# Kernel optimization log

Measured on AMD Instinct MI355X. Metric: run time of the kernel, lower is better.

Reference implementation:

```python
import jax, jax.numpy as jnp
import numpy as np

D_EMB = 512
TIME_HORIZON = 1024.0
SEP_FOR_GRIDS = 1.0


def _sinusoid(x, D):
    # x: [..., D], already divided by the 10000^(2*(i//2)/D) position vector.
    # even dims -> sin, odd dims -> cos (matches the torch in-place slicing)
    idx = jnp.arange(D)
    return jnp.where(idx % 2 == 0, jnp.sin(x), jnp.cos(x))


def setup_inputs() -> dict:
    key = jax.random.key(0)
    k1, k2, k3 = jax.random.split(key, 3)
    T, B, L, D = 2, 16, 2048, D_EMB
    # positive event timestamps in (0, time_horizon); strictly nonzero so pad mask == valid-by-length mask logic stays simple
    times = jax.random.uniform(k1, (T, B, L), dtype=jnp.float32) * TIME_HORIZON
    type_emb = jax.random.normal(k2, (T, D), dtype=jnp.float32)  # nn.Embedding weight
    real_len = jax.random.randint(k3, (T, B), 1, L)              # ragged valid lengths per type per sample
    return {"times": times, "type_emb": type_emb, "real_len": real_len}


def reference(times, type_emb, real_len):
    T, B, L = times.shape
    D = type_emb.shape[1]
    pos = jnp.power(jnp.float32(10000.0), 2.0 * (jnp.arange(D) // 2) / D)  # [D]

    # per-event embedding = (time sinusoid + type embedding) masked by nonzero-pad
    pad = (times != 0)[..., None]                                         # [T,B,L,1]
    emb = (_sinusoid(times[..., None] / pos, D) + type_emb[:, None, None, :]) * pad  # [T,B,L,D]
    emb = emb.transpose(1, 0, 2, 3).reshape(B, T * L, D)                  # [B, T*L, D]

    # grid queries: sinusoidal encoding of grid mid-times
    G = int(TIME_HORIZON / SEP_FOR_GRIDS)
    mid = (jnp.arange(G, dtype=jnp.float32) + 0.5) * SEP_FOR_GRIDS        # [G]
    q = _sinusoid(mid[:, None] / pos, D)                                  # [G,D]

    # dot-product scores vs grid queries, scaled
    scores = jnp.einsum('bnd,gd->bng', emb, q) / jnp.sqrt(jnp.float32(D)) # [B,T*L,G]

    # ragged validity: only first real_len events of each type block take part in softmax
    valid = jnp.arange(L)[None, None, :] < real_len[:, :, None]           # [T,B,L]
    valid = valid.transpose(1, 0, 2).reshape(B, T * L)                    # [B,T*L]

    # masked softmax over events (dim of concatenated valid events), weighted sum of embeddings
    w = jax.nn.softmax(jnp.where(valid[:, :, None], scores, -jnp.inf), axis=1)  # [B,T*L,G]
    return jnp.einsum('bng,bnd->bgd', w, emb)                             # [B,G,D]
```

## Files before the change

### kernel.cpp

```cpp
#include <hip/hip_runtime.h>
#include <hip/hip_bf16.h>
#include <math.h>

#define TT 2
#define BB 16
#define LL 2048
#define NN 4096
#define DD 512
#define GG 1024
#define SCALE 0.044194173824159216f
#define LOG2E 1.4426950408889634f
#define QSCL (SCALE * LOG2E)
#define C_IP 0.051905126482615036f

typedef unsigned short ushort_t;
typedef short short8 __attribute__((ext_vector_type(8)));
typedef float f32x4 __attribute__((ext_vector_type(4)));

__device__ __forceinline__ float inv_pos_f(int dhalf) {
    return exp2f(-C_IP * (float)dhalf);
}
__device__ __forceinline__ unsigned short f2b(float f) {
    union { float f; unsigned u; } x; x.f = f;
    unsigned r = x.u + 0x7fffu + ((x.u >> 16) & 1u);
    return (unsigned short)(r >> 16);
}
__device__ __forceinline__ float b2f(unsigned short u) {
    union { unsigned u; float f; } x; x.u = ((unsigned)u) << 16;
    return x.f;
}

__global__ void genT_kernel(const float* __restrict__ times,
                            const float* __restrict__ type_emb,
                            ushort_t* __restrict__ embT) {
    __shared__ float s_tm[64];
    __shared__ float s_te[DD];
    const int bid = blockIdx.x;
    const int b = bid >> 6;
    const int ntile = bid & 63;
    const int t = ntile >> 5;
    const int l0 = (ntile & 31) * 64;
    const int tid = threadIdx.x;

    if (tid < 64) s_tm[tid] = times[(size_t)(t * BB + b) * LL + l0 + tid];
    s_te[tid]       = type_emb[t * DD + tid];
    s_te[tid + 256] = type_emb[t * DD + tid + 256];
    __syncthreads();

    const int dsub = tid >> 3;
    const int nc = (tid & 7) * 8;
#pragma unroll 4
    for (int pass = 0; pass < 16; ++pass) {
        const int d = pass * 32 + dsub;
        const float ip = inv_pos_f(d >> 1);
        const float te = s_te[d];
        const bool use_cos = (d & 1);
        union { ushort_t us[8]; short8 v; } o;
#pragma unroll
        for (int j = 0; j < 8; ++j) {
            const float tm = s_tm[nc + j];
            const float th = tm * ip;
            const float v = use_cos ? __cosf(th) : __sinf(th);
            o.us[j] = f2b((v + te) * ((tm != 0.0f) ? 1.0f : 0.0f));
        }
        *reinterpret_cast<short8*>(
            embT + ((size_t)b * DD + d) * NN + (size_t)ntile * 64 + nc) = o.v;
    }
}

__global__ void ftab4_kernel(float* __restrict__ F4) {
    const int tid = threadIdx.x;
    const int e = blockIdx.x * 32 + (tid >> 3);
    const int jj = tid & 7;
    const float d0 = (float)e - 1024.0f;
    const float d1 = d0 + 1.0f;
    float F0 = 0.f, F1 = 0.f, D0 = 0.f, D1 = 0.f;
    for (int j = jj; j < 256; j += 8) {
        const float w = inv_pos_f(j);
        float s0, c0, s1, c1;
        __sincosf(d0 * w, &s0, &c0);
        __sincosf(d1 * w, &s1, &c1);
        F0 += c0; D0 -= w * s0;
        F1 += c1; D1 -= w * s1;
    }
#pragma unroll
    for (int off = 1; off < 8; off <<= 1) {
        F0 += __shfl_xor(F0, off, 64); F1 += __shfl_xor(F1, off, 64);
        D0 += __shfl_xor(D0, off, 64); D1 += __shfl_xor(D1, off, 64);
    }
    if (jj == 0) {
        const float cc = 3.f * (F1 - F0) - 2.f * D0 - D1;
        const float ee = 2.f * (F0 - F1) + D0 + D1;
        float4 v;
        v.x = F0 * QSCL; v.y = D0 * QSCL; v.z = cc * QSCL; v.w = ee * QSCL;
        reinterpret_cast<float4*>(F4)[e] = v;
    }
}

__global__ void gq_kernel(const float* __restrict__ type_emb, float* __restrict__ G) {
    const int g = blockIdx.x;
    const int tid = threadIdx.x;
    const float mid = (float)g + 0.5f;
    float a0 = 0.f, a1 = 0.f;
#pragma unroll
    for (int i = 0; i < 2; ++i) {
        const int d = i * 256 + tid;
        const float th = mid * inv_pos_f(d >> 1);
        const float v = (d & 1) ? cosf(th) : sinf(th);
        a0 += v * type_emb[d];
        a1 += v * type_emb[DD + d];
    }
#pragma unroll
    for (int off = 32; off; off >>= 1) {
        a0 += __shfl_xor(a0, off, 64);
        a1 += __shfl_xor(a1, off, 64);
    }
    __shared__ float r0[4], r1[4];
    const int wv = tid >> 6;
    if ((tid & 63) == 0) { r0[wv] = a0; r1[wv] = a1; }
    __syncthreads();
    if (tid == 0) {
        G[g]      = r0[0] + r0[1] + r0[2] + r0[3];
        G[GG + g] = r1[0] + r1[1] + r1[2] + r1[3];
    }
}

template <int NS>
__global__ __launch_bounds__(256, 2)
void attn5(const float* __restrict__ times,
           const ushort_t* __restrict__ embT,
           const float* __restrict__ Ft4,
           const float* __restrict__ Gt,
           const int* __restrict__ real_len,
           ushort_t* __restrict__ pO,
           float* __restrict__ pl) {
    __shared__ float4 sF[2048];
    __shared__ __align__(16) ushort_t sP[2][32 * 40];
    __shared__ float s_lred[2][32];

    constexpr int TPS = 128 / NS;
    const int idx = blockIdx.x;
    const int xcd = idx & 7;
    const int gt = (idx >> 3) & 31;
    const int hi = idx >> 8;
    const int b = xcd + ((hi & 1) << 3);
    const int s = hi >> 1;
    const int g0 = gt * 32;

    const int tid = threadIdx.x;
    const int lane = tid & 63;
    const int w = tid >> 6;
    const int l15 = lane & 15;
    const int quad = lane >> 4;
    const int mt1 = w >> 1;
    const int gt1 = w & 1;

    const int gme = g0 + gt1 * 16 + l15;
    const float gmid = (float)gme + 0.5f;
    const float c0 = Gt[gme] * QSCL - 4.0f;
    const float c1 = Gt[GG + gme] * QSCL - 4.0f;

    const ushort_t* embTB = embT + (size_t)b * DD * NN;

    const int rl0 = real_len[b];
    const int rl1 = real_len[BB + b];
    const int e0 = (rl0 + 31) >> 5;
    const int e1 = (rl1 + 31) >> 5;
    const int first = s * TPS;
    int count;
    if (first < 64) count = min(max(e0 - first, 0), TPS);
    else            count = min(max(64 + e1 - first, 0), TPS);

    f32x4 accO[8][2];
#pragma unroll
    for (int i = 0; i < 8; ++i) { accO[i][0] = (f32x4)0.f; accO[i][1] = (f32x4)0.f; }
    float ls = 0.f;

    short8 tf[8];
    auto prefetchT = [&](int nt) {
        const ushort_t* trow = embTB + (size_t)(w * 128 + l15) * NN + nt * 32 + quad * 8;
#pragma unroll
        for (int mt = 0; mt < 8; ++mt)
            tf[mt] = *reinterpret_cast<const short8*>(trow + (size_t)mt * 16 * NN);
    };
    auto times4 = [&](int nt) -> float4 {
        const int n = nt * 32 + mt1 * 16 + quad * 4;
        return *reinterpret_cast<const float4*>(
            times + (size_t)((n >> 11) * BB + b) * LL + (n & (LL - 1)));
    };

    float4 hv[4];
    float sr[4];
    auto gather = [&](float4 t4) {
        const float tt[4] = {t4.x, t4.y, t4.z, t4.w};
#pragma unroll
        for (int r = 0; r < 4; ++r) {
            const float u = (tt[r] - gmid) + 1024.0f;
            const int i = (int)u;
            sr[r] = u - (float)i;
            hv[r] = sF[i];
        }
    };

    if (count > 0) {
        const float4* Fg = reinterpret_cast<const float4*>(Ft4);
#pragma unroll
        for (int i = 0; i < 8; ++i) sF[tid + i * 256] = Fg[tid + i * 256];
        prefetchT(first);
        const float4 t40 = times4(first);
        __syncthreads();
        gather(t40);
    }
    float4 t4n;
    if (count > 1) t4n = times4(first + 1);

    for (int k = 0; k < count; ++k) {
        const int cur = first + k;
        const int buf = k & 1;

        const int nb = cur * 32 + mt1 * 16 + quad * 4;
        const int rl = (nb >= LL) ? rl1 : rl0;
        const float cc = (nb >= LL) ? c1 : c0;
        const int lb = nb & (LL - 1);
        float p[4];
#pragma unroll
        for (int r = 0; r < 4; ++r) {
            const float sv = sr[r];
            const float4 h = hv[r];
            const float Fv = h.x + sv * (h.y + sv * (h.z + sv * h.w));
            p[r] = (lb + r < rl) ? exp2f(Fv + cc) : 0.0f;
        }
        ls += (p[0] + p[1]) + (p[2] + p[3]);
        {
            union { unsigned short us[4]; unsigned long long u64; } pk;
            pk.us[0] = f2b(p[0]); pk.us[1] = f2b(p[1]); pk.us[2] = f2b(p[2]); pk.us[3] = f2b(p[3]);
            *reinterpret_cast<unsigned long long*>(
                sP[buf] + (gt1 * 16 + l15) * 40 + mt1 * 16 + quad * 4) = pk.u64;
        }

        asm volatile("s_waitcnt lgkmcnt(0)\n" ::: "memory");
        __builtin_amdgcn_s_barrier();

        if (k + 1 < count) {
            gather(t4n);
            if (k + 2 < count) t4n = times4(cur + 2);
        }

        {
            short8 bP0 = *reinterpret_cast<const short8*>(sP[buf] + l15 * 40 + quad * 8);
            short8 bP1 = *reinterpret_cast<const short8*>(sP[buf] + (16 + l15) * 40 + quad * 8);
            __builtin_amdgcn_s_setprio(1);
#pragma unroll
            for (int mt = 0; mt < 8; ++mt) {
                accO[mt][0] = __builtin_amdgcn_mfma_f32_16x16x32_bf16(tf[mt], bP0, accO[mt][0], 0, 0, 0);
                accO[mt][1] = __builtin_amdgcn_mfma_f32_16x16x32_bf16(tf[mt], bP1, accO[mt][1], 0, 0, 0);
            }
            __builtin_amdgcn_s_setprio(0);
        }
        if (k + 1 < count) prefetchT(cur + 1);
    }

    ls += __shfl_xor(ls, 16, 64);
    ls += __shfl_xor(ls, 32, 64);
    if (lane < 16) s_lred[mt1][gt1 * 16 + lane] = ls;
    __syncthreads();

    if (w == 0 && lane < 32)
        pl[((size_t)s * BB + b) * GG + g0 + lane] = s_lred[0][lane] + s_lred[1][lane];

    ushort_t* po = pO + (((size_t)s * BB + b) * GG) * DD;
#pragma unroll
    for (int mt = 0; mt < 8; ++mt) {
#pragma unroll
        for (int gtt = 0; gtt < 2; ++gtt) {
            union { unsigned short us[4]; unsigned long long u64; } pk;
            pk.us[0] = f2b(accO[mt][gtt][0]); pk.us[1] = f2b(accO[mt][gtt][1]);
            pk.us[2] = f2b(accO[mt][gtt][2]); pk.us[3] = f2b(accO[mt][gtt][3]);
            const int g = g0 + gtt * 16 + l15;
            const int d = w * 128 + mt * 16 + quad * 4;
            *reinterpret_cast<unsigned long long*>(po + (size_t)g * DD + d) = pk.u64;
        }
    }
}

template <int NS>
__global__ void combine3(const ushort_t* __restrict__ pO,
                         const float* __restrict__ pl,
                         float* __restrict__ out) {
    const size_t i4 = (size_t)blockIdx.x * 256 + threadIdx.x;
    const size_t base = i4 * 4;
    const size_t bg = base >> 9;
    float lsum = 0.f;
#pragma unroll
    for (int s = 0; s < NS; ++s) lsum += pl[(size_t)s * BB * GG + bg];
    const float inv = 1.0f / lsum;
    float o[4] = {0.f, 0.f, 0.f, 0.f};
#pragma unroll
    for (int s = 0; s < NS; ++s) {
        union { unsigned long long u64; unsigned short us[4]; } pk;
        pk.u64 = *reinterpret_cast<const unsigned long long*>(
            pO + (size_t)s * BB * GG * DD + base);
#pragma unroll
        for (int j = 0; j < 4; ++j) o[j] += b2f(pk.us[j]);
    }
    float4 v;
    v.x = o[0] * inv; v.y = o[1] * inv; v.z = o[2] * inv; v.w = o[3] * inv;
    *reinterpret_cast<float4*>(out + base) = v;
}

__global__ void emb_kernel(const float* __restrict__ times,
                           const float* __restrict__ type_emb,
                           ushort_t* __restrict__ emb) {
    const int row = blockIdx.x;
    const int b = row >> 12;
    const int n = row & (NN - 1);
    const int t = n >> 11;
    const int l = n & (LL - 1);
    const float tm = times[(size_t)(t * BB + b) * LL + l];
    const float pad = (tm != 0.0f) ? 1.0f : 0.0f;
    const int tid = threadIdx.x;
#pragma unroll
    for (int i = 0; i < 2; ++i) {
        int d = i * 256 + tid;
        float theta = tm * inv_pos_f(d >> 1);
        float v = (d & 1) ? cosf(theta) : sinf(theta);
        v = (v + type_emb[t * DD + d]) * pad;
        emb[(size_t)row * DD + d] = f2b(v);
    }
}
__global__ void qgrid_kernel(float* __restrict__ qbuf) {
    const int g = blockIdx.x;
    const int tid = threadIdx.x;
    const float mid = (float)g + 0.5f;
#pragma unroll
    for (int i = 0; i < 4; ++i) {
        int d = i * 128 + tid;
        float theta = mid * inv_pos_f(d >> 1);
        float v = (d & 1) ? cosf(theta) : sinf(theta);
        qbuf[(size_t)g * DD + d] = v;
    }
}
__global__ void attn_kernel(const ushort_t* __restrict__ emb,
                            const float* __restrict__ qbuf,
                            const int* __restrict__ real_len,
                            float* __restrict__ out) {
    __shared__ float s_lds[NN];
    __shared__ float q_s[DD];
    __shared__ float red[8];
    const int blk = blockIdx.x;
    const int b = blk >> 10;
    const int g = blk & (GG - 1);
    const int tid = threadIdx.x;
    const int lane = tid & 63;
    const int wave = tid >> 6;
    q_s[tid]       = qbuf[(size_t)g * DD + tid];
    q_s[tid + 256] = qbuf[(size_t)g * DD + tid + 256];
    __syncthreads();
    float qr[8];
#pragma unroll
    for (int j = 0; j < 8; ++j) qr[j] = q_s[lane * 8 + j];
    const unsigned int* embB =
        reinterpret_cast<const unsigned int*>(emb) + (size_t)b * NN * (DD / 2);
#pragma unroll 2
    for (int it = 0; it < NN / 4; ++it) {
        const int n = it * 4 + wave;
        const uint4 raw = *reinterpret_cast<const uint4*>(embB + (size_t)n * (DD / 2) + lane * 4);
        float sacc = 0.f;
        sacc = fmaf(__uint_as_float(raw.x << 16),         qr[0], sacc);
        sacc = fmaf(__uint_as_float(raw.x & 0xffff0000u), qr[1], sacc);
        sacc = fmaf(__uint_as_float(raw.y << 16),         qr[2], sacc);
        sacc = fmaf(__uint_as_float(raw.y & 0xffff0000u), qr[3], sacc);
        sacc = fmaf(__uint_as_float(raw.z << 16),         qr[4], sacc);
        sacc = fmaf(__uint_as_float(raw.z & 0xffff0000u), qr[5], sacc);
        sacc = fmaf(__uint_as_float(raw.w << 16),         qr[6], sacc);
        sacc = fmaf(__uint_as_float(raw.w & 0xffff0000u), qr[7], sacc);
#pragma unroll
        for (int off = 32; off; off >>= 1) sacc += __shfl_xor(sacc, off, 64);
        if (lane == 0) s_lds[n] = sacc * SCALE;
    }
    __syncthreads();
    const int rl0 = real_len[b];
    const int rl1 = real_len[BB + b];
    float m = -INFINITY;
    float sv[16];
#pragma unroll
    for (int i = 0; i < 16; ++i) {
        const int n = i * 256 + tid;
        float sc = s_lds[n];
        const int l = n & (LL - 1);
        const bool valid = l < ((n < LL) ? rl0 : rl1);
        sc = valid ? sc : -INFINITY;
        sv[i] = sc;
        m = fmaxf(m, sc);
    }
#pragma unroll
    for (int off = 32; off; off >>= 1) m = fmaxf(m, __shfl_xor(m, off, 64));
    if (lane == 0) red[wave] = m;
    __syncthreads();
    m = fmaxf(fmaxf(red[0], red[1]), fmaxf(red[2], red[3]));
    float lsum = 0.f;
#pragma unroll
    for (int i = 0; i < 16; ++i) {
        const int n = i * 256 + tid;
        const float e = expf(sv[i] - m);
        s_lds[n] = e;
        lsum += e;
    }
#pragma unroll
    for (int off = 32; off; off >>= 1) lsum += __shfl_xor(lsum, off, 64);
    if (lane == 0) red[4 + wave] = lsum;
    __syncthreads();
    const float inv_l = 1.0f / (red[4] + red[5] + red[6] + red[7]);
    float acc[8] = {0.f, 0.f, 0.f, 0.f, 0.f, 0.f, 0.f, 0.f};
#pragma unroll 2
    for (int kk = 0; kk < NN / 4; ++kk) {
        const int n = kk * 4 + wave;
        const float p = s_lds[n];
        const uint4 raw = *reinterpret_cast<const uint4*>(embB + (size_t)n * (DD / 2) + lane * 4);
        acc[0] = fmaf(p, __uint_as_float(raw.x << 16),         acc[0]);
        acc[1] = fmaf(p, __uint_as_float(raw.x & 0xffff0000u), acc[1]);
        acc[2] = fmaf(p, __uint_as_float(raw.y << 16),         acc[2]);
        acc[3] = fmaf(p, __uint_as_float(raw.y & 0xffff0000u), acc[3]);
        acc[4] = fmaf(p, __uint_as_float(raw.z << 16),         acc[4]);
        acc[5] = fmaf(p, __uint_as_float(raw.z & 0xffff0000u), acc[5]);
        acc[6] = fmaf(p, __uint_as_float(raw.w << 16),         acc[6]);
        acc[7] = fmaf(p, __uint_as_float(raw.w & 0xffff0000u), acc[7]);
    }
    __syncthreads();
    *reinterpret_cast<float4*>(&s_lds[wave * DD + lane * 8])     = make_float4(acc[0], acc[1], acc[2], acc[3]);
    *reinterpret_cast<float4*>(&s_lds[wave * DD + lane * 8 + 4]) = make_float4(acc[4], acc[5], acc[6], acc[7]);
    __syncthreads();
    {
        const int d0 = tid * 2;
        const float o0 = (s_lds[d0]     + s_lds[DD + d0]     + s_lds[2 * DD + d0]     + s_lds[3 * DD + d0])     * inv_l;
        const float o1 = (s_lds[d0 + 1] + s_lds[DD + d0 + 1] + s_lds[2 * DD + d0 + 1] + s_lds[3 * DD + d0 + 1]) * inv_l;
        *reinterpret_cast<float2*>(out + (size_t)blk * DD + d0) = make_float2(o0, o1);
    }
}

extern "C" void kernel_launch(void* const* d_in, const int* in_sizes, int n_in,
                              void* d_out, int out_size, void* d_ws, size_t ws_size,
                              hipStream_t stream) {
    const float* times    = (const float*)d_in[0];
    const float* type_emb = (const float*)d_in[1];
    const int*   real_len = (const int*)d_in[2];
    float* out = (float*)d_out;

    const size_t embTBytes = (size_t)BB * DD * NN * sizeof(ushort_t);
    const size_t tabBytes  = 64 * 1024;
    const size_t pOslice   = (size_t)BB * GG * DD * sizeof(ushort_t);
    const size_t plslice   = (size_t)BB * GG * sizeof(float);

    ushort_t* embT = (ushort_t*)d_ws;
    float* Ftab = (float*)((char*)d_ws + embTBytes);
    float* Gtab = (float*)((char*)d_ws + embTBytes + 32 * 1024);
    char* pbase = (char*)d_ws + embTBytes + tabBytes;

    auto need = [&](size_t ns) { return embTBytes + tabBytes + ns * (pOslice + plslice); };

    int NS = 0;
    if      (ws_size >= need(4)) NS = 4;
    else if (ws_size >= need(2)) NS = 2;

    if (NS > 0) {
        genT_kernel<<<BB * 64, 256, 0, stream>>>(times, type_emb, embT);
        ftab4_kernel<<<64, 256, 0, stream>>>(Ftab);
        gq_kernel<<<GG, 256, 0, stream>>>(type_emb, Gtab);
        ushort_t* pO = (ushort_t*)pbase;
        float* pl = (float*)(pbase + (size_t)NS * pOslice);
        if (NS == 4) {
            attn5<4><<<4 * 512, 256, 0, stream>>>(times, embT, Ftab, Gtab, real_len, pO, pl);
            combine3<4><<<(BB * GG * DD) / (256 * 4), 256, 0, stream>>>(pO, pl, out);
        } else {
            attn5<2><<<2 * 512, 256, 0, stream>>>(times, embT, Ftab, Gtab, real_len, pO, pl);
            combine3<2><<<(BB * GG * DD) / (256 * 4), 256, 0, stream>>>(pO, pl, out);
        }
    } else {
        ushort_t* emb = (ushort_t*)d_ws;
        float* qbuf = (float*)((char*)d_ws + embTBytes);
        emb_kernel<<<BB * NN, 256, 0, stream>>>(times, type_emb, emb);
        qgrid_kernel<<<GG, 128, 0, stream>>>(qbuf);
        attn_kernel<<<BB * GG, 256, 0, stream>>>(emb, qbuf, real_len, out);
    }
}
```

Baseline: 292.9 us.

## Repartition warps so each computes full P fragment in registers, removing LDS exchange

Each wave now computes all eight softmax weights of its MFMA B-operand for one 16-grid half directly in registers. Previously the four waves split the weights, exchanged them through shared memory and hit a barrier every tile. Each wave now covers 256 embedding dims with 16 accumulators instead of 128 dims across two grid halves. This removes the per-iteration LDS round trip and barrier, and the final shared-memory reduction of the row sums. In exchange the exp/polynomial work per wave doubles, since two waves recompute the same P, and register pressure rises with 16 tf prefetch registers at the same 2-block occupancy bound.

```diff
diff --git a/kernel.cpp b/kernel.cpp
--- a/kernel.cpp
+++ b/kernel.cpp
@@ -127,7 +127,7 @@
 
 template <int NS>
 __global__ __launch_bounds__(256, 2)
-void attn5(const float* __restrict__ times,
+void attn6(const float* __restrict__ times,
            const ushort_t* __restrict__ embT,
            const float* __restrict__ Ft4,
            const float* __restrict__ Gt,
@@ -135,8 +135,6 @@
            ushort_t* __restrict__ pO,
            float* __restrict__ pl) {
     __shared__ float4 sF[2048];
-    __shared__ __align__(16) ushort_t sP[2][32 * 40];
-    __shared__ float s_lred[2][32];
 
     constexpr int TPS = 128 / NS;
     const int idx = blockIdx.x;
@@ -152,10 +150,10 @@
     const int w = tid >> 6;
     const int l15 = lane & 15;
     const int quad = lane >> 4;
-    const int mt1 = w >> 1;
-    const int gt1 = w & 1;
-
-    const int gme = g0 + gt1 * 16 + l15;
+    const int dh = w & 1;
+    const int gh = w >> 1;
+
+    const int gme = g0 + gh * 16 + l15;
     const float gmid = (float)gme + 0.5f;
     const float c0 = Gt[gme] * QSCL - 4.0f;
     const float c1 = Gt[GG + gme] * QSCL - 4.0f;
@@ -171,30 +169,35 @@
     if (first < 64) count = min(max(e0 - first, 0), TPS);
     else            count = min(max(64 + e1 - first, 0), TPS);
 
-    f32x4 accO[8][2];
-#pragma unroll
-    for (int i = 0; i < 8; ++i) { accO[i][0] = (f32x4)0.f; accO[i][1] = (f32x4)0.f; }
+    f32x4 accO[16];
+#pragma unroll
+    for (int i = 0; i < 16; ++i) accO[i] = (f32x4)0.f;
     float ls = 0.f;
 
-    short8 tf[8];
+    short8 tf[16];
     auto prefetchT = [&](int nt) {
-        const ushort_t* trow = embTB + (size_t)(w * 128 + l15) * NN + nt * 32 + quad * 8;
-#pragma unroll
-        for (int mt = 0; mt < 8; ++mt)
+        const ushort_t* trow = embTB + (size_t)(dh * 256 + l15) * NN + nt * 32 + quad * 8;
+#pragma unroll
+        for (int mt = 0; mt < 16; ++mt)
             tf[mt] = *reinterpret_cast<const short8*>(trow + (size_t)mt * 16 * NN);
     };
-    auto times4 = [&](int nt) -> float4 {
-        const int n = nt * 32 + mt1 * 16 + quad * 4;
-        return *reinterpret_cast<const float4*>(
-            times + (size_t)((n >> 11) * BB + b) * LL + (n & (LL - 1)));
+    struct f8 { float4 a, b; };
+    auto times8 = [&](int nt) -> f8 {
+        const int n = nt * 32 + quad * 8;
+        const float* base = times + (size_t)((n >> 11) * BB + b) * LL + (n & (LL - 1));
+        f8 r;
+        r.a = *reinterpret_cast<const float4*>(base);
+        r.b = *reinterpret_cast<const float4*>(base + 4);
+        return r;
     };
 
-    float4 hv[4];
-    float sr[4];
-    auto gather = [&](float4 t4) {
-        const float tt[4] = {t4.x, t4.y, t4.z, t4.w};
-#pragma unroll
-        for (int r = 0; r < 4; ++r) {
+    float4 hv[8];
+    float sr[8];
+    auto gather = [&](f8 t8) {
+        const float tt[8] = {t8.a.x, t8.a.y, t8.a.z, t8.a.w,
+                             t8.b.x, t8.b.y, t8.b.z, t8.b.w};
+#pragma unroll
+        for (int r = 0; r < 8; ++r) {
             const float u = (tt[r] - gmid) + 1024.0f;
             const int i = (int)u;
             sr[r] = u - (float)i;
@@ -202,84 +205,67 @@
         }
     };
 
+    f8 t8n;
     if (count > 0) {
         const float4* Fg = reinterpret_cast<const float4*>(Ft4);
 #pragma unroll
         for (int i = 0; i < 8; ++i) sF[tid + i * 256] = Fg[tid + i * 256];
         prefetchT(first);
-        const float4 t40 = times4(first);
+        const f8 t80 = times8(first);
         __syncthreads();
-        gather(t40);
-    }
-    float4 t4n;
-    if (count > 1) t4n = times4(first + 1);
+        gather(t80);
+        if (count > 1) t8n = times8(first + 1);
+    }
 
     for (int k = 0; k < count; ++k) {
         const int cur = first + k;
-        const int buf = k & 1;
-
-        const int nb = cur * 32 + mt1 * 16 + quad * 4;
+
+        const int nb = cur * 32;
         const int rl = (nb >= LL) ? rl1 : rl0;
         const float cc = (nb >= LL) ? c1 : c0;
-        const int lb = nb & (LL - 1);
-        float p[4];
-#pragma unroll
-        for (int r = 0; r < 4; ++r) {
+        const int lb = (nb & (LL - 1)) + quad * 8;
+        float p[8];
+#pragma unroll
+        for (int r = 0; r < 8; ++r) {
             const float sv = sr[r];
             const float4 h = hv[r];
             const float Fv = h.x + sv * (h.y + sv * (h.z + sv * h.w));
             p[r] = (lb + r < rl) ? exp2f(Fv + cc) : 0.0f;
         }
-        ls += (p[0] + p[1]) + (p[2] + p[3]);
-        {
-            union { unsigned short us[4]; unsigned long long u64; } pk;
-            pk.us[0] = f2b(p[0]); pk.us[1] = f2b(p[1]); pk.us[2] = f2b(p[2]); pk.us[3] = f2b(p[3]);
-            *reinterpret_cast<unsigned long long*>(
-                sP[buf] + (gt1 * 16 + l15) * 40 + mt1 * 16 + quad * 4) = pk.u64;
+        ls += ((p[0] + p[1]) + (p[2] + p[3])) + ((p[4] + p[5]) + (p[6] + p[7]));
+
+        union { unsigned short us[8]; short8 v; } pk;
+#pragma unroll
+        for (int r = 0; r < 8; ++r) pk.us[r] = f2b(p[r]);
+        const short8 bP = pk.v;
+
+        if (k + 1 < count) {
+            gather(t8n);
+            if (k + 2 < count) t8n = times8(cur + 2);
         }
 
-        asm volatile("s_waitcnt lgkmcnt(0)\n" ::: "memory");
-        __builtin_amdgcn_s_barrier();
-
-        if (k + 1 < count) {
-            gather(t4n);
-            if (k + 2 < count) t4n = times4(cur + 2);
-        }
-
-        {
-            short8 bP0 = *reinterpret_cast<const short8*>(sP[buf] + l15 * 40 + quad * 8);
-            short8 bP1 = *reinterpret_cast<const short8*>(sP[buf] + (16 + l15) * 40 + quad * 8);
-            __builtin_amdgcn_s_setprio(1);
-#pragma unroll
-            for (int mt = 0; mt < 8; ++mt) {
-                accO[mt][0] = __builtin_amdgcn_mfma_f32_16x16x32_bf16(tf[mt], bP0, accO[mt][0], 0, 0, 0);
-                accO[mt][1] = __builtin_amdgcn_mfma_f32_16x16x32_bf16(tf[mt], bP1, accO[mt][1], 0, 0, 0);
-            }
-            __builtin_amdgcn_s_setprio(0);
-        }
+        __builtin_amdgcn_s_setprio(1);
+#pragma unroll
+        for (int mt = 0; mt < 16; ++mt)
+            accO[mt] = __builtin_amdgcn_mfma_f32_16x16x32_bf16(tf[mt], bP, accO[mt], 0, 0, 0);
+        __builtin_amdgcn_s_setprio(0);
+
         if (k + 1 < count) prefetchT(cur + 1);
     }
 
     ls += __shfl_xor(ls, 16, 64);
     ls += __shfl_xor(ls, 32, 64);
-    if (lane < 16) s_lred[mt1][gt1 * 16 + lane] = ls;
-    __syncthreads();
-
-    if (w == 0 && lane < 32)
-        pl[((size_t)s * BB + b) * GG + g0 + lane] = s_lred[0][lane] + s_lred[1][lane];
+    if (dh == 0 && lane < 16)
+        pl[((size_t)s * BB + b) * GG + gme] = ls;
 
     ushort_t* po = pO + (((size_t)s * BB + b) * GG) * DD;
 #pragma unroll
-    for (int mt = 0; mt < 8; ++mt) {
-#pragma unroll
-        for (int gtt = 0; gtt < 2; ++gtt) {
-            union { unsigned short us[4]; unsigned long long u64; } pk;
-            pk.us[0] = f2b(accO[mt][gtt][0]); pk.us[1] = f2b(accO[mt][gtt][1]);
-            pk.us[2] = f2b(accO[mt][gtt][2]); pk.us[3] = f2b(accO[mt][gtt][3]);
-            const int g = g0 + gtt * 16 + l15;
-            const int d = w * 128 + mt * 16 + quad * 4;
-            *reinterpret_cast<unsigned long long*>(po + (size_t)g * DD + d) = pk.u64;
-        }
+    for (int mt = 0; mt < 16; ++mt) {
+        union { unsigned short us[4]; unsigned long long u64; } pk2;
+        pk2.us[0] = f2b(accO[mt][0]); pk2.us[1] = f2b(accO[mt][1]);
+        pk2.us[2] = f2b(accO[mt][2]); pk2.us[3] = f2b(accO[mt][3]);
+        const int d = dh * 256 + mt * 16 + quad * 4;
+        *reinterpret_cast<unsigned long long*>(po + (size_t)gme * DD + d) = pk2.u64;
     }
 }
 
@@ -469,10 +455,10 @@
         ushort_t* pO = (ushort_t*)pbase;
         float* pl = (float*)(pbase + (size_t)NS * pOslice);
         if (NS == 4) {
-            attn5<4><<<4 * 512, 256, 0, stream>>>(times, embT, Ftab, Gtab, real_len, pO, pl);
+            attn6<4><<<4 * 512, 256, 0, stream>>>(times, embT, Ftab, Gtab, real_len, pO, pl);
             combine3<4><<<(BB * GG * DD) / (256 * 4), 256, 0, stream>>>(pO, pl, out);
         } else {
-            attn5<2><<<2 * 512, 256, 0, stream>>>(times, embT, Ftab, Gtab, real_len, pO, pl);
+            attn6<2><<<2 * 512, 256, 0, stream>>>(times, embT, Ftab, Gtab, real_len, pO, pl);
             combine3<2><<<(BB * GG * DD) / (256 * 4), 256, 0, stream>>>(pO, pl, out);
         }
     } else {
```

Result: slower. 439.2 us (+49.9%).

## Retile attention kernel to 64-grid blocks with 512 threads and 8 waves

Applied to the files above, without the earlier changes.

The attention kernel moves from 256-thread blocks covering 32 grid points with 4 waves to 512-thread blocks covering 64 grid points with 8 waves. Each wave now handles 64 of the D dimensions across 64 grid points, so it keeps 4x4 MFMA accumulators instead of 8x2. Each embedding fragment loaded from global memory is therefore reused across more grid columns, which roughly halves the redundant embT traffic per block and halves the number of blocks. The cost is more waves synchronising at each barrier and a different register and occupancy profile under launch_bounds(512,4).

```diff
diff --git a/kernel.cpp b/kernel.cpp
--- a/kernel.cpp
+++ b/kernel.cpp
@@ -126,39 +126,36 @@
 }
 
 template <int NS>
-__global__ __launch_bounds__(256, 2)
-void attn5(const float* __restrict__ times,
-           const ushort_t* __restrict__ embT,
-           const float* __restrict__ Ft4,
-           const float* __restrict__ Gt,
-           const int* __restrict__ real_len,
-           ushort_t* __restrict__ pO,
-           float* __restrict__ pl) {
+__global__ __launch_bounds__(512, 4)
+void attn11(const float* __restrict__ times,
+            const ushort_t* __restrict__ embT,
+            const float* __restrict__ Ft4,
+            const float* __restrict__ Gt,
+            const int* __restrict__ real_len,
+            ushort_t* __restrict__ pO,
+            float* __restrict__ pl) {
     __shared__ float4 sF[2048];
-    __shared__ __align__(16) ushort_t sP[2][32 * 40];
-    __shared__ float s_lred[2][32];
+    __shared__ __align__(16) ushort_t sP[2][64 * 40];
+    __shared__ float s_lp[8][64];
 
     constexpr int TPS = 128 / NS;
     const int idx = blockIdx.x;
     const int xcd = idx & 7;
-    const int gt = (idx >> 3) & 31;
-    const int hi = idx >> 8;
+    const int gt = (idx >> 3) & 15;
+    const int hi = idx >> 7;
     const int b = xcd + ((hi & 1) << 3);
     const int s = hi >> 1;
-    const int g0 = gt * 32;
+    const int g0 = gt * 64;
 
     const int tid = threadIdx.x;
     const int lane = tid & 63;
     const int w = tid >> 6;
     const int l15 = lane & 15;
     const int quad = lane >> 4;
-    const int mt1 = w >> 1;
-    const int gt1 = w & 1;
-
-    const int gme = g0 + gt1 * 16 + l15;
-    const float gmid = (float)gme + 0.5f;
-    const float c0 = Gt[gme] * QSCL - 4.0f;
-    const float c1 = Gt[GG + gme] * QSCL - 4.0f;
+
+    const float gmid = (float)(g0 + lane) + 0.5f;
+    const float c0 = Gt[g0 + lane] * QSCL - 4.0f;
+    const float c1 = Gt[GG + g0 + lane] * QSCL - 4.0f;
 
     const ushort_t* embTB = embT + (size_t)b * DD * NN;
 
@@ -171,20 +168,22 @@
     if (first < 64) count = min(max(e0 - first, 0), TPS);
     else            count = min(max(64 + e1 - first, 0), TPS);
 
-    f32x4 accO[8][2];
-#pragma unroll
-    for (int i = 0; i < 8; ++i) { accO[i][0] = (f32x4)0.f; accO[i][1] = (f32x4)0.f; }
+    f32x4 accO[4][4];
+#pragma unroll
+    for (int i = 0; i < 4; ++i)
+#pragma unroll
+        for (int j = 0; j < 4; ++j) accO[i][j] = (f32x4)0.f;
     float ls = 0.f;
 
-    short8 tf[8];
+    short8 tf[4];
     auto prefetchT = [&](int nt) {
-        const ushort_t* trow = embTB + (size_t)(w * 128 + l15) * NN + nt * 32 + quad * 8;
-#pragma unroll
-        for (int mt = 0; mt < 8; ++mt)
+        const ushort_t* trow = embTB + (size_t)(w * 64 + l15) * NN + nt * 32 + quad * 8;
+#pragma unroll
+        for (int mt = 0; mt < 4; ++mt)
             tf[mt] = *reinterpret_cast<const short8*>(trow + (size_t)mt * 16 * NN);
     };
     auto times4 = [&](int nt) -> float4 {
-        const int n = nt * 32 + mt1 * 16 + quad * 4;
+        const int n = nt * 32 + w * 4;
         return *reinterpret_cast<const float4*>(
             times + (size_t)((n >> 11) * BB + b) * LL + (n & (LL - 1)));
     };
@@ -205,7 +204,7 @@
     if (count > 0) {
         const float4* Fg = reinterpret_cast<const float4*>(Ft4);
 #pragma unroll
-        for (int i = 0; i < 8; ++i) sF[tid + i * 256] = Fg[tid + i * 256];
+        for (int i = 0; i < 4; ++i) sF[tid + i * 512] = Fg[tid + i * 512];
         prefetchT(first);
         const float4 t40 = times4(first);
         __syncthreads();
@@ -218,7 +217,7 @@
         const int cur = first + k;
         const int buf = k & 1;
 
-        const int nb = cur * 32 + mt1 * 16 + quad * 4;
+        const int nb = cur * 32 + w * 4;
         const int rl = (nb >= LL) ? rl1 : rl0;
         const float cc = (nb >= LL) ? c1 : c0;
         const int lb = nb & (LL - 1);
@@ -235,7 +234,7 @@
             union { unsigned short us[4]; unsigned long long u64; } pk;
             pk.us[0] = f2b(p[0]); pk.us[1] = f2b(p[1]); pk.us[2] = f2b(p[2]); pk.us[3] = f2b(p[3]);
             *reinterpret_cast<unsigned long long*>(
-                sP[buf] + (gt1 * 16 + l15) * 40 + mt1 * 16 + quad * 4) = pk.u64;
+                sP[buf] + lane * 40 + w * 4) = pk.u64;
         }
 
         asm volatile("s_waitcnt lgkmcnt(0)\n" ::: "memory");
@@ -247,37 +246,41 @@
         }
 
         {
-            short8 bP0 = *reinterpret_cast<const short8*>(sP[buf] + l15 * 40 + quad * 8);
-            short8 bP1 = *reinterpret_cast<const short8*>(sP[buf] + (16 + l15) * 40 + quad * 8);
+            short8 bP[4];
+#pragma unroll
+            for (int j = 0; j < 4; ++j)
+                bP[j] = *reinterpret_cast<const short8*>(sP[buf] + (j * 16 + l15) * 40 + quad * 8);
             __builtin_amdgcn_s_setprio(1);
 #pragma unroll
-            for (int mt = 0; mt < 8; ++mt) {
-                accO[mt][0] = __builtin_amdgcn_mfma_f32_16x16x32_bf16(tf[mt], bP0, accO[mt][0], 0, 0, 0);
-                accO[mt][1] = __builtin_amdgcn_mfma_f32_16x16x32_bf16(tf[mt], bP1, accO[mt][1], 0, 0, 0);
+            for (int mt = 0; mt < 4; ++mt) {
+#pragma unroll
+                for (int j = 0; j < 4; ++j)
+                    accO[mt][j] = __builtin_amdgcn_mfma_f32_16x16x32_bf16(tf[mt], bP[j], accO[mt][j], 0, 0, 0);
             }
             __builtin_amdgcn_s_setprio(0);
         }
         if (k + 1 < count) prefetchT(cur + 1);
     }
 
-    ls += __shfl_xor(ls, 16, 64);
-    ls += __shfl_xor(ls, 32, 64);
-    if (lane < 16) s_lred[mt1][gt1 * 16 + lane] = ls;
-    __syncthreads();
-
-    if (w == 0 && lane < 32)
-        pl[((size_t)s * BB + b) * GG + g0 + lane] = s_lred[0][lane] + s_lred[1][lane];
+    s_lp[w][lane] = ls;
+    __syncthreads();
+    if (tid < 64) {
+        float t = 0.f;
+#pragma unroll
+        for (int i = 0; i < 8; ++i) t += s_lp[i][tid];
+        pl[((size_t)s * BB + b) * GG + g0 + tid] = t;
+    }
 
     ushort_t* po = pO + (((size_t)s * BB + b) * GG) * DD;
 #pragma unroll
-    for (int mt = 0; mt < 8; ++mt) {
-#pragma unroll
-        for (int gtt = 0; gtt < 2; ++gtt) {
+    for (int mt = 0; mt < 4; ++mt) {
+#pragma unroll
+        for (int j = 0; j < 4; ++j) {
             union { unsigned short us[4]; unsigned long long u64; } pk;
-            pk.us[0] = f2b(accO[mt][gtt][0]); pk.us[1] = f2b(accO[mt][gtt][1]);
-            pk.us[2] = f2b(accO[mt][gtt][2]); pk.us[3] = f2b(accO[mt][gtt][3]);
-            const int g = g0 + gtt * 16 + l15;
-            const int d = w * 128 + mt * 16 + quad * 4;
+            pk.us[0] = f2b(accO[mt][j][0]); pk.us[1] = f2b(accO[mt][j][1]);
+            pk.us[2] = f2b(accO[mt][j][2]); pk.us[3] = f2b(accO[mt][j][3]);
+            const int g = g0 + j * 16 + l15;
+            const int d = w * 64 + mt * 16 + quad * 4;
             *reinterpret_cast<unsigned long long*>(po + (size_t)g * DD + d) = pk.u64;
         }
     }
@@ -469,10 +472,10 @@
         ushort_t* pO = (ushort_t*)pbase;
         float* pl = (float*)(pbase + (size_t)NS * pOslice);
         if (NS == 4) {
-            attn5<4><<<4 * 512, 256, 0, stream>>>(times, embT, Ftab, Gtab, real_len, pO, pl);
+            attn11<4><<<8 * 16 * 8, 512, 0, stream>>>(times, embT, Ftab, Gtab, real_len, pO, pl);
             combine3<4><<<(BB * GG * DD) / (256 * 4), 256, 0, stream>>>(pO, pl, out);
         } else {
-            attn5<2><<<2 * 512, 256, 0, stream>>>(times, embT, Ftab, Gtab, real_len, pO, pl);
+            attn11<2><<<8 * 16 * 4, 512, 0, stream>>>(times, embT, Ftab, Gtab, real_len, pO, pl);
             combine3<2><<<(BB * GG * DD) / (256 * 4), 256, 0, stream>>>(pO, pl, out);
         }
     } else {
```

Result: slower. 350.3 us (+19.6%).
